# Kernel optimization log

Hardware: AMD Instinct MI355X
Metric: run time of the kernel (lower is better)

Reference implementation:

```python
import jax, jax.numpy as jnp
import numpy as np

N = 50000   # nodes
E = 800000  # edges (avg degree 16)
D = 64      # node_feature_dim == node_embedding_dim
L = 4       # num_layers
G = 64      # number of graphs in the batch


def setup_inputs() -> dict:
    key = jax.random.key(0)
    ks = jax.random.split(key, 6)
    x = jax.random.normal(ks[0], (N, D), dtype=jnp.float32)
    edge_index = jax.random.randint(ks[1], (2, E), 0, N, dtype=jnp.int32)
    batch = jnp.sort(jax.random.randint(ks[2], (N,), 0, G, dtype=jnp.int32))
    scale = 1.0 / np.sqrt(D)
    conv_W = jax.random.normal(ks[3], (L, D, D), dtype=jnp.float32) * scale
    conv_b = jnp.zeros((L, D), dtype=jnp.float32)
    lin_W = jax.random.normal(ks[4], (D, 1), dtype=jnp.float32) * scale
    lin_b = jnp.zeros((1,), dtype=jnp.float32)
    return dict(x=x, conv_W=conv_W, conv_b=conv_b, lin_W=lin_W, lin_b=lin_b,
                edge_index=edge_index, batch=batch)


def reference(x, conv_W, conv_b, lin_W, lin_b, edge_index, batch):
    n = x.shape[0]
    # GCNConv: add self-loops, symmetric deg^{-1/2} normalization (computed once; graph is static)
    loop = jnp.arange(n, dtype=edge_index.dtype)
    src = jnp.concatenate([edge_index[0], loop])
    dst = jnp.concatenate([edge_index[1], loop])
    deg = jax.ops.segment_sum(jnp.ones_like(dst, dtype=x.dtype), dst, num_segments=n)
    dinv = jnp.where(deg > 0, jax.lax.rsqrt(deg), 0.0)
    norm = (dinv[src] * dinv[dst])[:, None]  # [E+N, 1]
    # stacked GCNConv + ReLU
    for l in range(conv_W.shape[0]):
        h = x @ conv_W[l]                                       # [N, D] linear transform
        agg = jax.ops.segment_sum(norm * h[src], dst, num_segments=n)  # gather-normalize-scatter
        x = jax.nn.relu(agg + conv_b[l])
    # global_mean_pool over graphs
    counts = jax.ops.segment_sum(jnp.ones((n,), x.dtype), batch, num_segments=G)
    sums = jax.ops.segment_sum(x, batch, num_segments=G)        # [G, D]
    pooled = sums / jnp.maximum(counts, 1.0)[:, None]
    return pooled @ lin_W + lin_b                               # [G, 1]
```

## Files before the change

kernel.cpp:

```cpp
#include <hip/hip_runtime.h>
#include <hip/hip_fp16.h>


#define D 64
#define BSHIFT 10
#define BNODES 1024
#define EPT 16
#define CB (256 * EPT)
#define CAP 24576
#define SW(r, c4) ((c4) ^ (((r) >> 2) & 15))


__global__ __launch_bounds__(256) void setup_kernel(
        const float* __restrict__ W, float* __restrict__ Wt,
        int* __restrict__ bcnt, int L) {
    int b = blockIdx.x;
    if (b < L) {
        const float* w = W + (size_t)b * D * D;
        float* wt = Wt + (size_t)b * D * D;
        for (int idx = threadIdx.x; idx < D * D; idx += 256) {
            int k = idx >> 6, c = idx & 63;
            wt[c * D + k] = w[idx];
        }
    } else {
        bcnt[threadIdx.x] = 0;
    }
}


__global__ __launch_bounds__(256) void partition_kernel(
        const int* __restrict__ src, const int* __restrict__ dst,
        int* __restrict__ bcnt, unsigned* __restrict__ eb, int e) {
    __shared__ int cB[256], gb[256], cur[256];
    int t = threadIdx.x;
    cB[t] = 0;
    __syncthreads();
    int base = blockIdx.x * CB;
    int ps[EPT], pd[EPT];
    #pragma unroll
    for (int k = 0; k < EPT; ++k) {
        int i = base + t + k * 256;
        if (i < e) {
            ps[k] = src[i];
            pd[k] = dst[i];
            atomicAdd(&cB[pd[k] >> BSHIFT], 1);
        } else {
            pd[k] = -1;
        }
    }
    __syncthreads();
    if (cB[t]) gb[t] = atomicAdd(&bcnt[t], cB[t]);
    cur[t] = 0;
    __syncthreads();
    #pragma unroll
    for (int k = 0; k < EPT; ++k) {
        if (pd[k] >= 0) {
            int b = pd[k] >> BSHIFT;
            int p = atomicAdd(&cur[b], 1);
            eb[(size_t)b * CAP + gb[b] + p] =
                (unsigned)(ps[k] & 0xFFFF) | ((unsigned)(pd[k] & (BNODES - 1)) << 16);
        }
    }
}

__global__ __launch_bounds__(BNODES) void build_csr(
        const unsigned* __restrict__ eb, const int* __restrict__ bcnt,
        int* __restrict__ row_start, float* __restrict__ dinv,
        int* __restrict__ csr_src, int n, int e) {
    __shared__ int sh[BNODES];
    __shared__ int cur[BNODES];
    __shared__ int boffsh;
    int b = blockIdx.x, t = threadIdx.x;
    if (t == 0) boffsh = 0;
    __syncthreads();
    if (t < b) atomicAdd(&boffsh, bcnt[t]);
    int cnt = bcnt[b];
    const unsigned* ebb = eb + (size_t)b * CAP;
    sh[t] = 0;
    __syncthreads();
    int boff = boffsh;
    for (int i = t; i < cnt; i += BNODES) atomicAdd(&sh[ebb[i] >> 16], 1);
    __syncthreads();
    int c = sh[t];
    __syncthreads();
    for (int off = 1; off < BNODES; off <<= 1) {
        int vp = (t >= off) ? sh[t - off] : 0;
        __syncthreads();
        sh[t] += vp;
        __syncthreads();
    }
    int a = sh[t] - c + boff;
    int node = b * BNODES + t;
    if (node < n) {
        row_start[node] = a;
        dinv[node] = 1.0f / sqrtf((float)(c + 1));
    }
    if (b == 0 && t == 0) row_start[n] = e;
    cur[t] = a;
    __syncthreads();
    for (int i = t; i < cnt; i += BNODES) {
        unsigned v = ebb[i];
        int p = atomicAdd(&cur[v >> 16], 1);
        csr_src[p] = (int)(v & 0xFFFFu);
    }
}


__global__ __launch_bounds__(256, 3) void matmul_kernel(
        const float* __restrict__ X, const float* __restrict__ Wt,
        const float* __restrict__ dinv, __half* __restrict__ H, int n) {
    __shared__ float4 Xs[64 * 16];
    __shared__ float4 Ws[64 * 16];
    int t = threadIdx.x;
    int rowBase = blockIdx.x * 64;
    const float4* X4 = (const float4*)X;
    const float4* Wt4 = (const float4*)Wt;
    #pragma unroll
    for (int p = 0; p < 4; ++p) {
        int rl = (t >> 4) + 16 * p;
        int c4 = t & 15;
        int r = rowBase + rl;
        float4 v = make_float4(0.f, 0.f, 0.f, 0.f);
        if (r < n) v = X4[(size_t)r * 16 + c4];
        Xs[rl * 16 + SW(rl, c4)] = v;
        Ws[rl * 16 + SW(rl, c4)] = Wt4[rl * 16 + c4];
    }
    __syncthreads();
    int wv = t >> 6, lane = t & 63;
    int rg = lane >> 2, cg = lane & 3;
    int r0 = rg * 4;
    int c0 = wv * 16 + cg * 4;
    float acc[4][4] = {};
    #pragma unroll 2
    for (int k4 = 0; k4 < 16; ++k4) {
        float4 xv[4], wvv[4];
        #pragma unroll
        for (int i = 0; i < 4; ++i) xv[i] = Xs[(r0 + i) * 16 + SW(r0 + i, k4)];
        #pragma unroll
        for (int j = 0; j < 4; ++j) wvv[j] = Ws[(c0 + j) * 16 + SW(c0 + j, k4)];
        #pragma unroll
        for (int i = 0; i < 4; ++i)
            #pragma unroll
            for (int j = 0; j < 4; ++j) {
                acc[i][j] += xv[i].x * wvv[j].x;
                acc[i][j] += xv[i].y * wvv[j].y;
                acc[i][j] += xv[i].z * wvv[j].z;
                acc[i][j] += xv[i].w * wvv[j].w;
            }
    }
    #pragma unroll
    for (int i = 0; i < 4; ++i) {
        int r = rowBase + r0 + i;
        if (r < n) {
            float dr = dinv[r];
            ushort4 o;
            o.x = __half_as_ushort(__float2half(dr * acc[i][0]));
            o.y = __half_as_ushort(__float2half(dr * acc[i][1]));
            o.z = __half_as_ushort(__float2half(dr * acc[i][2]));
            o.w = __half_as_ushort(__float2half(dr * acc[i][3]));
            *(ushort4*)&H[(size_t)r * D + c0] = o;
        }
    }
}


__global__ __launch_bounds__(256) void agg_fused(
        const __half* __restrict__ H, const int* __restrict__ csr_src,
        const int* __restrict__ row_start, const float* __restrict__ dinv,
        const float* __restrict__ bias, const float* __restrict__ Wtn,
        __half* __restrict__ out, int n) {
    __shared__ float4 Wsh4[D * 16];
    __shared__ float rowsh[4][D];
    int t = threadIdx.x;
    {
        const float4* Wt4 = (const float4*)Wtn;
        #pragma unroll
        for (int p = 0; p < 4; ++p) {
            int i = t + p * 256;
            int c = i >> 4, k4 = i & 15;
            Wsh4[(c << 4) | (k4 ^ (c & 15))] = Wt4[i];
        }
    }
    __syncthreads();
    int wave = t >> 6, lane = t & 63;
    int v = blockIdx.x * 4 + wave;
    bool active = v < n;
    float dv = 0.f, o = 0.f;
    if (active) {
        dv = dinv[v];
        float acc = __half2float(H[(size_t)v * D + lane]);
        int s = row_start[v];
        int e = row_start[v + 1];
        int i = s;
        #pragma unroll 1
        for (; i + 16 <= e; i += 16) {
            int u[16];
            float h[16];
            #pragma unroll
            for (int k = 0; k < 16; ++k) u[k] = csr_src[i + k];
            #pragma unroll
            for (int k = 0; k < 16; ++k) h[k] = __half2float(H[(size_t)u[k] * D + lane]);
            #pragma unroll
            for (int k = 0; k < 16; ++k) acc += h[k];
        }
        #pragma unroll 1
        for (; i + 4 <= e; i += 4) {
            int u0 = csr_src[i + 0], u1 = csr_src[i + 1];
            int u2 = csr_src[i + 2], u3 = csr_src[i + 3];
            float h0 = __half2float(H[(size_t)u0 * D + lane]);
            float h1 = __half2float(H[(size_t)u1 * D + lane]);
            float h2 = __half2float(H[(size_t)u2 * D + lane]);
            float h3 = __half2float(H[(size_t)u3 * D + lane]);
            acc += h0;
            acc += h1;
            acc += h2;
            acc += h3;
        }
        for (; i < e; ++i) {
            int u = csr_src[i];
            acc += __half2float(H[(size_t)u * D + lane]);
        }
        o = fmaxf(dv * acc + bias[lane], 0.f);
    }
    rowsh[wave][lane] = o;
    if (active) {
        const float4* r4p = (const float4*)&rowsh[wave][0];
        float accT = 0.f;
        #pragma unroll
        for (int k4 = 0; k4 < 16; ++k4) {
            float4 r = r4p[k4];
            float4 w = Wsh4[(lane << 4) | (k4 ^ (lane & 15))];
            accT += r.x * w.x;
            accT += r.y * w.y;
            accT += r.z * w.z;
            accT += r.w * w.w;
        }
        out[(size_t)v * D + lane] = __float2half(dv * accT);
    }
}


__global__ __launch_bounds__(256) void agg_kernel(
        const __half* __restrict__ H, const int* __restrict__ csr_src,
        const int* __restrict__ row_start, const float* __restrict__ dinv,
        const float* __restrict__ bias, float* __restrict__ out, int n) {
    int wave = threadIdx.x >> 6, lane = threadIdx.x & 63;
    int v = blockIdx.x * 4 + wave;
    if (v >= n) return;
    float dv = dinv[v];
    float acc = __half2float(H[(size_t)v * D + lane]);
    int s = row_start[v];
    int e = row_start[v + 1];
    int i = s;
    #pragma unroll 1
    for (; i + 16 <= e; i += 16) {
        int u[16];
        float h[16];
        #pragma unroll
        for (int k = 0; k < 16; ++k) u[k] = csr_src[i + k];
        #pragma unroll
        for (int k = 0; k < 16; ++k) h[k] = __half2float(H[(size_t)u[k] * D + lane]);
        #pragma unroll
        for (int k = 0; k < 16; ++k) acc += h[k];
    }
    #pragma unroll 1
    for (; i + 4 <= e; i += 4) {
        int u0 = csr_src[i + 0], u1 = csr_src[i + 1];
        int u2 = csr_src[i + 2], u3 = csr_src[i + 3];
        float h0 = __half2float(H[(size_t)u0 * D + lane]);
        float h1 = __half2float(H[(size_t)u1 * D + lane]);
        float h2 = __half2float(H[(size_t)u2 * D + lane]);
        float h3 = __half2float(H[(size_t)u3 * D + lane]);
        acc += h0;
        acc += h1;
        acc += h2;
        acc += h3;
    }
    for (; i < e; ++i) {
        int u = csr_src[i];
        acc += __half2float(H[(size_t)u * D + lane]);
    }
    out[(size_t)v * D + lane] = fmaxf(dv * acc + bias[lane], 0.f);
}


__device__ __forceinline__ int lower_bound_g(const int* __restrict__ b, int n, int g) {
    int lo = 0, hi = n;
    while (lo < hi) { int m = (lo + hi) >> 1; if (b[m] < g) lo = m + 1; else hi = m; }
    return lo;
}

__global__ __launch_bounds__(1024) void pool_final(
        const float* __restrict__ X, const int* __restrict__ batch,
        const float* __restrict__ linW, const float* __restrict__ linb,
        float* __restrict__ out, int n) {
    __shared__ float sh[16][64];
    int g = blockIdx.x;
    int gs = lower_bound_g(batch, n, g);
    int ge = lower_bound_g(batch, n, g + 1);
    int wv = threadIdx.x >> 6, lane = threadIdx.x & 63;
    float acc = 0.f;
    for (int r = gs + wv; r < ge; r += 16)
        acc += X[(size_t)r * D + lane];
    sh[wv][lane] = acc;
    __syncthreads();
    if (wv == 0) {
        float tot = 0.f;
        #pragma unroll
        for (int i = 0; i < 16; ++i) tot += sh[i][lane];
        float cnt = fmaxf((float)(ge - gs), 1.f);
        float p = (tot / cnt) * linW[lane];
        #pragma unroll
        for (int off = 32; off > 0; off >>= 1) p += __shfl_down(p, off, 64);
        if (lane == 0) out[g] = p + linb[0];
    }
}


extern "C" void kernel_launch(void* const* d_in, const int* in_sizes, int n_in,
                              void* d_out, int out_size, void* d_ws, size_t ws_size,
                              hipStream_t stream) {
    const float* x      = (const float*)d_in[0];
    const float* conv_W = (const float*)d_in[1];
    const float* conv_b = (const float*)d_in[2];
    const float* lin_W  = (const float*)d_in[3];
    const float* lin_b  = (const float*)d_in[4];
    const int*   edge   = (const int*)d_in[5];
    const int*   batch  = (const int*)d_in[6];

    const int n = in_sizes[0] / D;
    const int e = in_sizes[5] / 2;
    const int L = in_sizes[1] / (D * D);
    const int G = out_size;

    const int* esrc = edge;
    const int* edst = edge + e;

    char* ws = (char*)d_ws;
    size_t off = 0;
    auto alloc = [&](size_t bytes) -> void* {
        void* p = ws + off;
        off += (bytes + 255) & ~(size_t)255;
        return p;
    };
    const int nb = (n + BNODES - 1) / BNODES;
    int*    bcnt      = (int*)alloc(256 * 4);
    float*  dinv      = (float*)alloc((size_t)n * 4);
    int*    row_start = (int*)alloc((size_t)(n + 1) * 4);
    int*    csr_src   = (int*)alloc((size_t)e * 4);
    float*  wtbuf     = (float*)alloc((size_t)L * D * D * 4);
    __half* h16a      = (__half*)alloc((size_t)n * D * 2);
    __half* h16b      = (__half*)alloc((size_t)n * D * 2);
    float*  hf32      = (float*)alloc((size_t)n * D * 4);
    unsigned* eb      = (unsigned*)hf32;
    (void)ws_size;

    setup_kernel<<<L + 1, 256, 0, stream>>>(conv_W, wtbuf, bcnt, L);

    const int pb = (e + CB - 1) / CB;
    partition_kernel<<<pb, 256, 0, stream>>>(esrc, edst, bcnt, eb, e);
    build_csr       <<<nb, BNODES, 0, stream>>>(eb, bcnt, row_start, dinv,
                                                csr_src, n, e);

    const int ablocks = (n + 3) / 4;

    matmul_kernel<<<(n + 63) / 64, 256, 0, stream>>>(x, wtbuf, dinv, h16a, n);
    agg_fused<<<ablocks, 256, 0, stream>>>(h16a, csr_src, row_start, dinv,
                                           conv_b + 0 * D, wtbuf + 1 * D * D, h16b, n);
    agg_fused<<<ablocks, 256, 0, stream>>>(h16b, csr_src, row_start, dinv,
                                           conv_b + 1 * D, wtbuf + 2 * D * D, h16a, n);
    agg_fused<<<ablocks, 256, 0, stream>>>(h16a, csr_src, row_start, dinv,
                                           conv_b + 2 * D, wtbuf + 3 * D * D, h16b, n);
    agg_kernel<<<ablocks, 256, 0, stream>>>(h16b, csr_src, row_start, dinv,
                                            conv_b + 3 * D, hf32, n);

    pool_final<<<G, 1024, 0, stream>>>(hf32, batch, lin_W, lin_b, (float*)d_out, n);
}
```

Baseline: 206.1 us.

## Split each wave into two half-waves gathering alternate neighbors with half2 loads

The neighbor gather in both aggregation kernels now has each half of the 64-lane wave process alternate edges. Each lane loads a __half2 (two features), so one half-wave reads a full 128-byte row. Neighbor indices are loaded cooperatively, 32 at a time, and broadcast with shuffles instead of each lane reading them separately. The two half-wave partial sums are combined with a shuffle-xor, and the self-loop term and bias are applied once at the end. The goal is twice as many independent row loads in flight, wider loads and fewer index loads, at the cost of predicated-off slots when a node's degree is not a multiple of 32 and of half the wave sitting idle during the epilogue.

```diff
diff --git a/kernel.cpp b/kernel.cpp
--- a/kernel.cpp
+++ b/kernel.cpp
@@ -164,13 +164,45 @@
 }
 
 
+__device__ __forceinline__ float2 gather_sum(
+        const __half2* __restrict__ H2, const int* __restrict__ csr_src,
+        int s, int deg, int half, int f2) {
+    float2 acc = make_float2(0.f, 0.f);
+    int li = (half << 5) - 32 + f2;
+    (void)li;
+    for (int base = 0; base < deg; base += 32) {
+        int rem = deg - base;
+        int idx = 0;
+        int lj = f2;
+        if (lj < rem) idx = csr_src[s + base + lj];
+        float2 h[16];
+        #pragma unroll
+        for (int ii = 0; ii < 16; ++ii) {
+            int el = 2 * ii + half;
+            int u = __shfl(idx, el & 31, 64);
+            if (el < rem) {
+                h[ii] = __half22float2(H2[(size_t)u * 32 + f2]);
+            } else {
+                h[ii] = make_float2(0.f, 0.f);
+            }
+        }
+        #pragma unroll
+        for (int ii = 0; ii < 16; ++ii) {
+            acc.x += h[ii].x;
+            acc.y += h[ii].y;
+        }
+    }
+    return acc;
+}
+
+
 __global__ __launch_bounds__(256) void agg_fused(
         const __half* __restrict__ H, const int* __restrict__ csr_src,
         const int* __restrict__ row_start, const float* __restrict__ dinv,
         const float* __restrict__ bias, const float* __restrict__ Wtn,
         __half* __restrict__ out, int n) {
     __shared__ float4 Wsh4[D * 16];
-    __shared__ float rowsh[4][D];
+    __shared__ __align__(16) float2 rowsh[4][32];
     int t = threadIdx.x;
     {
         const float4* Wt4 = (const float4*)Wtn;
@@ -183,46 +215,28 @@
     }
     __syncthreads();
     int wave = t >> 6, lane = t & 63;
+    int half = lane >> 5, f2 = lane & 31;
     int v = blockIdx.x * 4 + wave;
     bool active = v < n;
-    float dv = 0.f, o = 0.f;
+    const __half2* H2 = (const __half2*)H;
+    float dv = 0.f;
+    float2 acc = make_float2(0.f, 0.f);
     if (active) {
         dv = dinv[v];
-        float acc = __half2float(H[(size_t)v * D + lane]);
         int s = row_start[v];
-        int e = row_start[v + 1];
-        int i = s;
-        #pragma unroll 1
-        for (; i + 16 <= e; i += 16) {
-            int u[16];
-            float h[16];
-            #pragma unroll
-            for (int k = 0; k < 16; ++k) u[k] = csr_src[i + k];
-            #pragma unroll
-            for (int k = 0; k < 16; ++k) h[k] = __half2float(H[(size_t)u[k] * D + lane]);
-            #pragma unroll
-            for (int k = 0; k < 16; ++k) acc += h[k];
-        }
-        #pragma unroll 1
-        for (; i + 4 <= e; i += 4) {
-            int u0 = csr_src[i + 0], u1 = csr_src[i + 1];
-            int u2 = csr_src[i + 2], u3 = csr_src[i + 3];
-            float h0 = __half2float(H[(size_t)u0 * D + lane]);
-            float h1 = __half2float(H[(size_t)u1 * D + lane]);
-            float h2 = __half2float(H[(size_t)u2 * D + lane]);
-            float h3 = __half2float(H[(size_t)u3 * D + lane]);
-            acc += h0;
-            acc += h1;
-            acc += h2;
-            acc += h3;
-        }
-        for (; i < e; ++i) {
-            int u = csr_src[i];
-            acc += __half2float(H[(size_t)u * D + lane]);
-        }
-        o = fmaxf(dv * acc + bias[lane], 0.f);
-    }
-    rowsh[wave][lane] = o;
+        int deg = row_start[v + 1] - s;
+        acc = gather_sum(H2, csr_src, s, deg, half, f2);
+    }
+    acc.x += __shfl_xor(acc.x, 32, 64);
+    acc.y += __shfl_xor(acc.y, 32, 64);
+    if (active && half == 0) {
+        float2 self = __half22float2(H2[(size_t)v * 32 + f2]);
+        float2 b2 = ((const float2*)bias)[f2];
+        float2 o;
+        o.x = fmaxf(dv * (self.x + acc.x) + b2.x, 0.f);
+        o.y = fmaxf(dv * (self.y + acc.y) + b2.y, 0.f);
+        rowsh[wave][f2] = o;
+    }
     if (active) {
         const float4* r4p = (const float4*)&rowsh[wave][0];
         float accT = 0.f;
@@ -244,43 +258,26 @@
         const __half* __restrict__ H, const int* __restrict__ csr_src,
         const int* __restrict__ row_start, const float* __restrict__ dinv,
         const float* __restrict__ bias, float* __restrict__ out, int n) {
-    int wave = threadIdx.x >> 6, lane = threadIdx.x & 63;
+    int t = threadIdx.x;
+    int wave = t >> 6, lane = t & 63;
+    int half = lane >> 5, f2 = lane & 31;
     int v = blockIdx.x * 4 + wave;
     if (v >= n) return;
+    const __half2* H2 = (const __half2*)H;
     float dv = dinv[v];
-    float acc = __half2float(H[(size_t)v * D + lane]);
     int s = row_start[v];
-    int e = row_start[v + 1];
-    int i = s;
-    #pragma unroll 1
-    for (; i + 16 <= e; i += 16) {
-        int u[16];
-        float h[16];
-        #pragma unroll
-        for (int k = 0; k < 16; ++k) u[k] = csr_src[i + k];
-        #pragma unroll
-        for (int k = 0; k < 16; ++k) h[k] = __half2float(H[(size_t)u[k] * D + lane]);
-        #pragma unroll
-        for (int k = 0; k < 16; ++k) acc += h[k];
-    }
-    #pragma unroll 1
-    for (; i + 4 <= e; i += 4) {
-        int u0 = csr_src[i + 0], u1 = csr_src[i + 1];
-        int u2 = csr_src[i + 2], u3 = csr_src[i + 3];
-        float h0 = __half2float(H[(size_t)u0 * D + lane]);
-        float h1 = __half2float(H[(size_t)u1 * D + lane]);
-        float h2 = __half2float(H[(size_t)u2 * D + lane]);
-        float h3 = __half2float(H[(size_t)u3 * D + lane]);
-        acc += h0;
-        acc += h1;
-        acc += h2;
-        acc += h3;
-    }
-    for (; i < e; ++i) {
-        int u = csr_src[i];
-        acc += __half2float(H[(size_t)u * D + lane]);
-    }
-    out[(size_t)v * D + lane] = fmaxf(dv * acc + bias[lane], 0.f);
+    int deg = row_start[v + 1] - s;
+    float2 acc = gather_sum(H2, csr_src, s, deg, half, f2);
+    acc.x += __shfl_xor(acc.x, 32, 64);
+    acc.y += __shfl_xor(acc.y, 32, 64);
+    if (half == 0) {
+        float2 self = __half22float2(H2[(size_t)v * 32 + f2]);
+        float2 b2 = ((const float2*)bias)[f2];
+        float2 o;
+        o.x = fmaxf(dv * (self.x + acc.x) + b2.x, 0.f);
+        o.y = fmaxf(dv * (self.y + acc.y) + b2.y, 0.f);
+        ((float2*)out)[(size_t)v * 32 + f2] = o;
+    }
 }
 
 
```

New measurement: 295.6 us. 43.4% more time.
